# Performance work log

Measured on AMD Instinct MI355X. Metric: run time of the kernel, lower is better.

The kernel has to match this reference:

```python
import jax, jax.numpy as jnp
import numpy as np

SCALE = 1.0  # module scale
# dropout is treated as identity (eval mode / deterministic reference)

def setup_inputs() -> dict:
    key = jax.random.key(0)
    k_x, k_w, k1, k2, k3 = jax.random.split(key, 5)
    B, S, D = 4, 4096, 1280
    x = jax.random.normal(k_x, (B, S, D), dtype=jnp.float32)
    W = jax.random.normal(k_w, (D, D), dtype=jnp.float32) * 0.02  # linear.weight [out, in]
    # kron factors are initialized to identity in the module; perturb slightly
    # so the rotation is non-trivial for correctness testing.
    kron_1 = jnp.eye(4, dtype=jnp.float32) + 0.01 * jax.random.normal(k1, (4, 4), dtype=jnp.float32)
    kron_2 = jnp.eye(8, dtype=jnp.float32) + 0.01 * jax.random.normal(k2, (8, 8), dtype=jnp.float32)
    kron_3 = jnp.eye(40, dtype=jnp.float32) + 0.01 * jax.random.normal(k3, (40, 40), dtype=jnp.float32)
    return {"x": x, "W": W, "kron_1": kron_1, "kron_2": kron_2, "kron_3": kron_3}

def reference(x, W, kron_1, kron_2, kron_3):
    # rotate_matrix = kron(kron(k1, k2), k3)  -> [in, in] = [1280, 1280]
    R = jnp.kron(jnp.kron(kron_1, kron_2), kron_3)
    # rotated_weight = (R @ W^T)^T ; F.linear(x, rotated_weight) = x @ (R @ W^T)
    rotated_weight = (R @ W.T).T  # [out, in]
    out = jnp.einsum('bsd,od->bso', x, rotated_weight)
    return out * SCALE
```

## Files before the change

kernel.cpp:

```cpp
#include <hip/hip_runtime.h>
#include <hip/hip_bf16.h>
#include <stdint.h>

typedef __bf16 bf16x8 __attribute__((ext_vector_type(8)));
typedef float floatx4 __attribute__((ext_vector_type(4)));

__device__ __forceinline__ void async_copy16(void* lds, const void* g) {
    __builtin_amdgcn_global_load_lds(
        (const __attribute__((address_space(1))) unsigned int*)g,
        (__attribute__((address_space(3))) unsigned int*)lds,
        16, 0, 0);
}

__global__ __launch_bounds__(256)
void prep(const float* __restrict__ x,
          const float* __restrict__ W,
          const float* __restrict__ K1,
          const float* __restrict__ K2,
          const float* __restrict__ K3,
          __hip_bfloat16* __restrict__ x_bf,
          __hip_bfloat16* __restrict__ Wrot,
          int nConv) {
    const int tid = threadIdx.x;

    if ((int)blockIdx.x < nConv) {
        const size_t i = ((size_t)blockIdx.x * 256 + tid) * 8;
        const float4 a = *(const float4*)(x + i);
        const float4 b = *(const float4*)(x + i + 4);
        bf16x8 v;
        v[0] = (__bf16)a.x; v[1] = (__bf16)a.y; v[2] = (__bf16)a.z; v[3] = (__bf16)a.w;
        v[4] = (__bf16)b.x; v[5] = (__bf16)b.y; v[6] = (__bf16)b.z; v[7] = (__bf16)b.w;
        *(bf16x8*)((__bf16*)x_bf + i) = v;
        return;
    }

    const int o = blockIdx.x - nConv;
    __shared__ __align__(16) float w0[1280];
    __shared__ __align__(16) float t1[1280];
    __shared__ __align__(16) float k3s[1600];
    __shared__ float k2s[64];
    __shared__ float k1s[16];

    for (int i = tid; i < 1280; i += 256) w0[i] = W[o * 1280 + i];
    for (int i = tid; i < 1600; i += 256) k3s[i] = K3[i];
    if (tid < 64) k2s[tid] = K2[tid];
    if (tid < 16) k1s[tid] = K1[tid];
    __syncthreads();

    for (int i = tid; i < 1280; i += 256) {
        const int p = i / 40, d3 = i % 40;
        const float4* w4 = (const float4*)(w0 + p * 40);
        const float4* k4 = (const float4*)(k3s + d3 * 40);
        float acc = 0.f;
#pragma unroll
        for (int t = 0; t < 10; ++t) {
            const float4 a = w4[t], b = k4[t];
            acc += a.x * b.x + a.y * b.y + a.z * b.z + a.w * b.w;
        }
        t1[i] = acc;
    }
    __syncthreads();

    for (int i = tid; i < 1280; i += 256) {
        const int d3 = i % 40, pd = i / 40;
        const int k1 = pd >> 3, d2 = pd & 7;
        float acc = 0.f;
#pragma unroll
        for (int k2 = 0; k2 < 8; ++k2) acc += t1[(k1 * 8 + k2) * 40 + d3] * k2s[d2 * 8 + k2];
        w0[i] = acc;
    }
    __syncthreads();

    for (int i = tid; i < 1280; i += 256) {
        const int d3 = i % 40, pd = i / 40;
        const int d1 = pd >> 3, d2 = pd & 7;
        float acc = 0.f;
#pragma unroll
        for (int k1 = 0; k1 < 4; ++k1) acc += w0[(k1 * 8 + d2) * 40 + d3] * k1s[d1 * 4 + k1];
        Wrot[(size_t)o * 1280 + i] = __float2bfloat16(acc);
    }
}

#define BM 256
#define BN 320
#define BK 64
#define AGRAN 2048
#define BGRAN 2560

__global__ __launch_bounds__(512, 2)
void gemm_bt(const __hip_bfloat16* __restrict__ A,
             const __hip_bfloat16* __restrict__ B,
             float* __restrict__ C,
             int M, int N, int K) {
    __shared__ bf16x8 As[2][AGRAN];
    __shared__ bf16x8 Bs[2][BGRAN];

    const int tid  = threadIdx.x;
    const int wave = tid >> 6;
    const int lane = tid & 63;
    const int q    = lane >> 4;
    const int r16  = lane & 15;
    const int wm   = wave >> 2;
    const int wn   = wave & 3;

    const int nTilesN = N / BN;
    const int chunkM  = (M / BM) >> 3;
    const int xcd = blockIdx.x & 7;
    const int s   = blockIdx.x >> 3;
    const int bm  = xcd * chunkM + s / nTilesN;
    const int bn  = s % nTilesN;
    const int tileM = bm * BM, tileN = bn * BN;

    uint32_t aoff[4], boff[5];
#pragma unroll
    for (int c = 0; c < 4; ++c) {
        const int g = c * 512 + tid;
        const int m = g >> 3, kv = (g & 7) ^ (m & 7);
        aoff[c] = (uint32_t)(((tileM + m) * K + kv * 8) * 2);
    }
#pragma unroll
    for (int c = 0; c < 5; ++c) {
        const int g = c * 512 + tid;
        const int m = g >> 3, kv = (g & 7) ^ (m & 7);
        boff[c] = (uint32_t)(((tileN + m) * K + kv * 8) * 2);
    }
    const char* Abase = (const char*)A;
    const char* Bbase = (const char*)B;

    int ai[8], bi[5];
#pragma unroll
    for (int i = 0; i < 8; ++i) {
        const int m = wm * 128 + i * 16 + r16;
        ai[i] = m * 8 + (q ^ (m & 7));
    }
#pragma unroll
    for (int j = 0; j < 5; ++j) {
        const int n = wn * 80 + j * 16 + r16;
        bi[j] = n * 8 + (q ^ (n & 7));
    }

    floatx4 acc[8][5];
#pragma unroll
    for (int i = 0; i < 8; ++i)
#pragma unroll
        for (int j = 0; j < 5; ++j) acc[i][j] = (floatx4){0.f, 0.f, 0.f, 0.f};

    const int nk = K / BK;

#pragma unroll
    for (int c = 0; c < 4; ++c)
        async_copy16(&As[0][c * 512 + wave * 64], Abase + aoff[c]);
#pragma unroll
    for (int c = 0; c < 5; ++c)
        async_copy16(&Bs[0][c * 512 + wave * 64], Bbase + boff[c]);
    asm volatile("s_waitcnt vmcnt(0)" ::: "memory");
    __builtin_amdgcn_s_barrier();

    for (int t = 0; t < nk; ++t) {
        const int cur = t & 1, nxt = cur ^ 1;
        const uint32_t kb = (uint32_t)((t + 1) * BK * 2);
        const bool hn = (t + 1 < nk);

        if (hn) {
#pragma unroll
            for (int c = 0; c < 4; ++c)
                async_copy16(&As[nxt][c * 512 + wave * 64], Abase + aoff[c] + kb);
#pragma unroll
            for (int c = 0; c < 5; ++c)
                async_copy16(&Bs[nxt][c * 512 + wave * 64], Bbase + boff[c] + kb);
        }

        bf16x8 af0[8], bf0[5];
#pragma unroll
        for (int i = 0; i < 8; ++i) af0[i] = As[cur][ai[i]];
#pragma unroll
        for (int j = 0; j < 5; ++j) bf0[j] = Bs[cur][bi[j]];

        __builtin_amdgcn_s_setprio(1);
#pragma unroll
        for (int i = 0; i < 8; ++i)
#pragma unroll
            for (int j = 0; j < 5; ++j)
                acc[i][j] = __builtin_amdgcn_mfma_f32_16x16x32_bf16(
                    af0[i], bf0[j], acc[i][j], 0, 0, 0);
        __builtin_amdgcn_s_setprio(0);

        bf16x8 af1[8], bf1[5];
#pragma unroll
        for (int i = 0; i < 8; ++i) af1[i] = As[cur][ai[i] ^ 4];
#pragma unroll
        for (int j = 0; j < 5; ++j) bf1[j] = Bs[cur][bi[j] ^ 4];

        __builtin_amdgcn_s_setprio(1);
#pragma unroll
        for (int i = 0; i < 8; ++i)
#pragma unroll
            for (int j = 0; j < 5; ++j)
                acc[i][j] = __builtin_amdgcn_mfma_f32_16x16x32_bf16(
                    af1[i], bf1[j], acc[i][j], 0, 0, 0);
        __builtin_amdgcn_s_setprio(0);

        if (hn) {
            asm volatile("s_waitcnt vmcnt(0)" ::: "memory");
            __builtin_amdgcn_sched_barrier(0);
            __builtin_amdgcn_s_barrier();
            __builtin_amdgcn_sched_barrier(0);
        }
    }

#pragma unroll
    for (int i = 0; i < 8; ++i) {
#pragma unroll
        for (int j = 0; j < 5; ++j) {
            const int col = tileN + wn * 80 + j * 16 + r16;
#pragma unroll
            for (int r = 0; r < 4; ++r) {
                const int row = tileM + wm * 128 + i * 16 + q * 4 + r;
                C[(size_t)row * N + col] = acc[i][j][r];
            }
        }
    }
}

extern "C" void kernel_launch(void* const* d_in, const int* in_sizes, int n_in,
                              void* d_out, int out_size, void* d_ws, size_t ws_size,
                              hipStream_t stream) {
    const float* x  = (const float*)d_in[0];
    const float* W  = (const float*)d_in[1];
    const float* K1 = (const float*)d_in[2];
    const float* K2 = (const float*)d_in[3];
    const float* K3 = (const float*)d_in[4];
    float* out = (float*)d_out;

    const int D = 1280;
    const int M = in_sizes[0] / D;
    const int N = D, K = D;

    __hip_bfloat16* x_bf = (__hip_bfloat16*)d_ws;
    __hip_bfloat16* Wrot = x_bf + (size_t)M * K;

    const int nConv = (M * K) / (256 * 8);
    prep<<<nConv + D, 256, 0, stream>>>(x, W, K1, K2, K3, x_bf, Wrot, nConv);
    gemm_bt<<<(M / BM) * (N / BN), 512, 0, stream>>>(x_bf, Wrot, out, M, N, K);
}
```

Before: 225.7 us.

## Load A fragments directly from global into registers, keep only B in LDS

The A operand is no longer staged through shared memory. Each wave loads its A fragments straight from global memory into registers, prefetching the next half-tile during the MFMA loop. The wave layout changes from 2x4 to 4x2, so each wave owns 64 rows by 160 columns. The vmcnt wait is relaxed so the in-flight A loads can overlap, and the next B fragments are read right after the barrier. This cuts LDS traffic and space but issues uncoalesced 16-byte global loads for A. The launch bound drops to one block per CU.

After: 333.0 us. +47.6%, slower.

```diff
diff --git a/kernel.cpp b/kernel.cpp
--- a/kernel.cpp
+++ b/kernel.cpp
@@ -84,15 +84,13 @@
 #define BM 256
 #define BN 320
 #define BK 64
-#define AGRAN 2048
 #define BGRAN 2560
 
-__global__ __launch_bounds__(512, 2)
+__global__ __launch_bounds__(512, 1)
 void gemm_bt(const __hip_bfloat16* __restrict__ A,
              const __hip_bfloat16* __restrict__ B,
              float* __restrict__ C,
              int M, int N, int K) {
-    __shared__ bf16x8 As[2][AGRAN];
     __shared__ bf16x8 Bs[2][BGRAN];
 
     const int tid  = threadIdx.x;
@@ -100,8 +98,8 @@
     const int lane = tid & 63;
     const int q    = lane >> 4;
     const int r16  = lane & 15;
-    const int wm   = wave >> 2;
-    const int wn   = wave & 3;
+    const int wm   = wave >> 1;
+    const int wn   = wave & 1;
 
     const int nTilesN = N / BN;
     const int chunkM  = (M / BM) >> 3;
@@ -111,111 +109,111 @@
     const int bn  = s % nTilesN;
     const int tileM = bm * BM, tileN = bn * BN;
 
-    uint32_t aoff[4], boff[5];
-#pragma unroll
-    for (int c = 0; c < 4; ++c) {
-        const int g = c * 512 + tid;
-        const int m = g >> 3, kv = (g & 7) ^ (m & 7);
-        aoff[c] = (uint32_t)(((tileM + m) * K + kv * 8) * 2);
-    }
+    uint32_t boff[5];
 #pragma unroll
     for (int c = 0; c < 5; ++c) {
         const int g = c * 512 + tid;
         const int m = g >> 3, kv = (g & 7) ^ (m & 7);
         boff[c] = (uint32_t)(((tileN + m) * K + kv * 8) * 2);
     }
-    const char* Abase = (const char*)A;
     const char* Bbase = (const char*)B;
 
-    int ai[8], bi[5];
-#pragma unroll
-    for (int i = 0; i < 8; ++i) {
-        const int m = wm * 128 + i * 16 + r16;
-        ai[i] = m * 8 + (q ^ (m & 7));
-    }
-#pragma unroll
-    for (int j = 0; j < 5; ++j) {
-        const int n = wn * 80 + j * 16 + r16;
+    int bi[10];
+#pragma unroll
+    for (int j = 0; j < 10; ++j) {
+        const int n = wn * 160 + j * 16 + r16;
         bi[j] = n * 8 + (q ^ (n & 7));
     }
 
-    floatx4 acc[8][5];
-#pragma unroll
-    for (int i = 0; i < 8; ++i)
-#pragma unroll
-        for (int j = 0; j < 5; ++j) acc[i][j] = (floatx4){0.f, 0.f, 0.f, 0.f};
+    const __hip_bfloat16* aptr[4];
+#pragma unroll
+    for (int i = 0; i < 4; ++i) {
+        const int row = tileM + wm * 64 + i * 16 + r16;
+        aptr[i] = A + (size_t)row * K + q * 8;
+    }
+
+    floatx4 acc[4][10];
+#pragma unroll
+    for (int i = 0; i < 4; ++i)
+#pragma unroll
+        for (int j = 0; j < 10; ++j) acc[i][j] = (floatx4){0.f, 0.f, 0.f, 0.f};
 
     const int nk = K / BK;
 
-#pragma unroll
-    for (int c = 0; c < 4; ++c)
-        async_copy16(&As[0][c * 512 + wave * 64], Abase + aoff[c]);
 #pragma unroll
     for (int c = 0; c < 5; ++c)
         async_copy16(&Bs[0][c * 512 + wave * 64], Bbase + boff[c]);
+
+    bf16x8 afA[4], afB[4], bf0[10], bf1[10];
+#pragma unroll
+    for (int i = 0; i < 4; ++i) afA[i] = *(const bf16x8*)(aptr[i]);
+
     asm volatile("s_waitcnt vmcnt(0)" ::: "memory");
     __builtin_amdgcn_s_barrier();
+#pragma unroll
+    for (int j = 0; j < 10; ++j) bf0[j] = Bs[0][bi[j]];
 
     for (int t = 0; t < nk; ++t) {
         const int cur = t & 1, nxt = cur ^ 1;
         const uint32_t kb = (uint32_t)((t + 1) * BK * 2);
         const bool hn = (t + 1 < nk);
 
+#pragma unroll
+        for (int i = 0; i < 4; ++i)
+            afB[i] = *(const bf16x8*)(aptr[i] + t * BK + 32);
         if (hn) {
-#pragma unroll
-            for (int c = 0; c < 4; ++c)
-                async_copy16(&As[nxt][c * 512 + wave * 64], Abase + aoff[c] + kb);
 #pragma unroll
             for (int c = 0; c < 5; ++c)
                 async_copy16(&Bs[nxt][c * 512 + wave * 64], Bbase + boff[c] + kb);
         }
-
-        bf16x8 af0[8], bf0[5];
-#pragma unroll
-        for (int i = 0; i < 8; ++i) af0[i] = As[cur][ai[i]];
-#pragma unroll
-        for (int j = 0; j < 5; ++j) bf0[j] = Bs[cur][bi[j]];
-
+        __builtin_amdgcn_sched_barrier(0);
         __builtin_amdgcn_s_setprio(1);
 #pragma unroll
-        for (int i = 0; i < 8; ++i)
-#pragma unroll
-            for (int j = 0; j < 5; ++j)
+        for (int j = 0; j < 10; ++j)
+#pragma unroll
+            for (int i = 0; i < 4; ++i)
                 acc[i][j] = __builtin_amdgcn_mfma_f32_16x16x32_bf16(
-                    af0[i], bf0[j], acc[i][j], 0, 0, 0);
+                    afA[i], bf0[j], acc[i][j], 0, 0, 0);
         __builtin_amdgcn_s_setprio(0);
-
-        bf16x8 af1[8], bf1[5];
-#pragma unroll
-        for (int i = 0; i < 8; ++i) af1[i] = As[cur][ai[i] ^ 4];
-#pragma unroll
-        for (int j = 0; j < 5; ++j) bf1[j] = Bs[cur][bi[j] ^ 4];
-
+        __builtin_amdgcn_sched_barrier(0);
+
+        if (hn) {
+#pragma unroll
+            for (int i = 0; i < 4; ++i)
+                afA[i] = *(const bf16x8*)(aptr[i] + (t + 1) * BK);
+        }
+#pragma unroll
+        for (int j = 0; j < 10; ++j) bf1[j] = Bs[cur][bi[j] ^ 4];
+        __builtin_amdgcn_sched_barrier(0);
         __builtin_amdgcn_s_setprio(1);
 #pragma unroll
-        for (int i = 0; i < 8; ++i)
-#pragma unroll
-            for (int j = 0; j < 5; ++j)
+        for (int j = 0; j < 10; ++j)
+#pragma unroll
+            for (int i = 0; i < 4; ++i)
                 acc[i][j] = __builtin_amdgcn_mfma_f32_16x16x32_bf16(
-                    af1[i], bf1[j], acc[i][j], 0, 0, 0);
+                    afB[i], bf1[j], acc[i][j], 0, 0, 0);
         __builtin_amdgcn_s_setprio(0);
+        __builtin_amdgcn_sched_barrier(0);
 
         if (hn) {
-            asm volatile("s_waitcnt vmcnt(0)" ::: "memory");
+            asm volatile("s_waitcnt vmcnt(4)" ::: "memory");
             __builtin_amdgcn_sched_barrier(0);
             __builtin_amdgcn_s_barrier();
             __builtin_amdgcn_sched_barrier(0);
-        }
-    }
-
-#pragma unroll
-    for (int i = 0; i < 8; ++i) {
-#pragma unroll
-        for (int j = 0; j < 5; ++j) {
-            const int col = tileN + wn * 80 + j * 16 + r16;
+#pragma unroll
+            for (int j = 0; j < 10; ++j) bf0[j] = Bs[nxt][bi[j]];
+            __builtin_amdgcn_sched_barrier(0);
+        }
+    }
+
+#pragma unroll
+    for (int i = 0; i < 4; ++i) {
+#pragma unroll
+        for (int j = 0; j < 10; ++j) {
+            const int col = tileN + wn * 160 + j * 16 + r16;
 #pragma unroll
             for (int r = 0; r < 4; ++r) {
-                const int row = tileM + wm * 128 + i * 16 + q * 4 + r;
+                const int row = tileM + wm * 64 + i * 16 + q * 4 + r;
                 C[(size_t)row * N + col] = acc[i][j][r];
             }
         }
```
